# Kernel tuning notes

Measured on AMD Instinct MI355X. Metric: run time of the kernel, lower is better.

The kernel has to match this reference:

```python
import jax, jax.numpy as jnp
import numpy as np

# Brevitas-style fake quantization:
#  - Int8ActPerTensorFloat: signed, symmetric, per-tensor float scale, range [-128, 127]
#  - 4-bit weight, narrow range: [-7, 7]
#  - Int32Bias: quantized at scale s_in * s_w
# Scales are taken from per-tensor abs-max statistics (brevitas stats-based init).

def _round(v):
    return jnp.round(v)

def _fake_quant(v, scale, qmin, qmax):
    return jnp.clip(_round(v / scale), qmin, qmax) * scale


def setup_inputs() -> dict:
    key = jax.random.key(0)
    k1, k2, k3 = jax.random.split(key, 3)
    x = jax.random.normal(k1, (16, 3, 224, 224), dtype=jnp.float32)
    W = jax.random.normal(k2, (128, 3, 3, 3), dtype=jnp.float32) * 0.1
    b = jax.random.normal(k3, (128,), dtype=jnp.float32) * 0.01
    return {"x": x, "W": W, "b": b}


def reference(x, W, b):
    EPS = 1e-8
    # input quant: int8 per-tensor
    s_in = jnp.maximum(jnp.max(jnp.abs(x)) / 127.0, EPS)
    x_q = _fake_quant(x, s_in, -128.0, 127.0)
    # weight quant: 4-bit narrow-range per-tensor
    s_w = jnp.maximum(jnp.max(jnp.abs(W)) / 7.0, EPS)
    w_q = _fake_quant(W, s_w, -7.0, 7.0)
    # bias quant: int32 at scale s_in * s_w
    s_b = s_in * s_w
    b_q = _fake_quant(b, s_b, -2147483648.0, 2147483647.0)
    # conv2d, NCHW x OIHW -> NCHW, stride 1, valid padding (torch default padding=0)
    y = jax.lax.conv_general_dilated(
        x_q, w_q, window_strides=(1, 1), padding="VALID",
        dimension_numbers=("NCHW", "OIHW", "NCHW"))
    y = y + b_q[None, :, None, None]
    # output quant: int8 per-tensor
    s_out = jnp.maximum(jnp.max(jnp.abs(y)) / 127.0, EPS)
    y_q = _fake_quant(y, s_out, -128.0, 127.0)
    return y_q
```

## Files before the change

### kernel.cpp

```cpp
#include <hip/hip_runtime.h>
#include <stdint.h>

#define QEPS 1e-8f


__global__ void k_init(unsigned int* s) { if (threadIdx.x < 4) s[threadIdx.x] = 0u; }

__global__ __launch_bounds__(256) void k_absmax(
    const float4* __restrict__ x, int n4,
    const float* __restrict__ W, int nw,
    unsigned int* __restrict__ s) {
  __shared__ unsigned int red[256];
  const int t = threadIdx.x;
  unsigned int m = 0u;
  const int i = blockIdx.x * 256 + t;
  if (i < n4) {
    float4 v = x[i];
    m =        __float_as_uint(v.x) & 0x7fffffffu;
    m = max(m, __float_as_uint(v.y) & 0x7fffffffu);
    m = max(m, __float_as_uint(v.z) & 0x7fffffffu);
    m = max(m, __float_as_uint(v.w) & 0x7fffffffu);
  }
  red[t] = m;
  __syncthreads();
  for (int off = 128; off > 0; off >>= 1) {
    if (t < off) red[t] = max(red[t], red[t + off]);
    __syncthreads();
  }
  if (t == 0) atomicMax(&s[0], red[0]);

  if (blockIdx.x == 0) {
    unsigned int mw = 0u;
    for (int j = t; j < nw; j += 256)
      mw = max(mw, __float_as_uint(W[j]) & 0x7fffffffu);
    __syncthreads();
    red[t] = mw;
    __syncthreads();
    for (int off = 128; off > 0; off >>= 1) {
      if (t < off) red[t] = max(red[t], red[t + off]);
      __syncthreads();
    }
    if (t == 0) atomicMax(&s[1], red[0]);
  }
}

template<int PASS>
__global__ __launch_bounds__(256, 3) void k_conv(
    const float* __restrict__ x, const float* __restrict__ W,
    const float* __restrict__ b, float* __restrict__ out,
    unsigned int* __restrict__ s) {
  __shared__ __align__(16) float wl[27][128];
  __shared__ __align__(16) float xl[9][132];
  __shared__ float redf[256];

  const int t = threadIdx.x;
  const int lane = t & 15;
  const int oc0 = (t >> 4) * 8;

  const float s_in = fmaxf(__uint_as_float(s[0]) / 127.0f, QEPS);
  const float s_w  = fmaxf(__uint_as_float(s[1]) / 7.0f,  QEPS);
  const float s_b  = s_in * s_w;

  float s_out = 1.0f, h = 1.0f;
  if (PASS == 1) {
    const float vmax = __uint_as_float(s[2]);
    s_out = fmaxf((s_b * vmax) / 127.0f, QEPS);
    h = s_b / s_out;
  }

  for (int i = t; i < 3456; i += 256) {
    const int o = i / 27;
    const int k = i - o * 27;
    float q = rintf(W[i] / s_w);
    wl[k][o] = fminf(fmaxf(q, -7.0f), 7.0f);
  }

  float qb[8];
  #pragma unroll
  for (int cc = 0; cc < 8; ++cc)
    qb[cc] = rintf(b[oc0 + cc] / s_b);

  float vmax_local = 0.0f;

  for (int it = 0; it < 4; ++it) {
    const int tile = blockIdx.x + it * 1776;
    const int owt = tile & 1;
    const int r2 = tile >> 1;
    const int n  = r2 & 15;
    const int oh = r2 >> 4;
    const int ow0 = owt * 128;

    for (int i = t; i < 9 * 132; i += 256) {
      const int row = i / 132;
      const int col = i - row * 132;
      const int c  = row / 3;
      const int kh = row - c * 3;
      const int gcol = ow0 + col;
      float q = 0.0f;
      if (gcol < 224) {
        const float xv = x[((n * 3 + c) * 224 + (oh + kh)) * 224 + gcol];
        q = fminf(fmaxf(rintf(xv / s_in), -128.0f), 127.0f);
      }
      xl[row][col] = q;
    }
    __syncthreads();

    float acc[8][8];
    #pragma unroll
    for (int r = 0; r < 8; ++r)
      #pragma unroll
      for (int cc = 0; cc < 8; ++cc) acc[r][cc] = 0.0f;

    #pragma unroll 1
    for (int ck = 0; ck < 9; ++ck) {
      const float* xr = &xl[ck][lane * 8];
      const float4 a0 = *(const float4*)xr;
      const float4 a1 = *(const float4*)(xr + 4);
      const float4 a2 = *(const float4*)(xr + 8);
      const float xw[12] = {a0.x, a0.y, a0.z, a0.w, a1.x, a1.y, a1.z, a1.w,
                            a2.x, a2.y, a2.z, a2.w};
      #pragma unroll
      for (int kw = 0; kw < 3; ++kw) {
        const float* wp = &wl[ck * 3 + kw][oc0];
        const float4 w0 = *(const float4*)wp;
        const float4 w1 = *(const float4*)(wp + 4);
        const float wv[8] = {w0.x, w0.y, w0.z, w0.w, w1.x, w1.y, w1.z, w1.w};
        #pragma unroll
        for (int r = 0; r < 8; ++r) {
          #pragma unroll
          for (int cc = 0; cc < 8; ++cc)
            acc[r][cc] += xw[r + kw] * wv[cc];
        }
      }
    }

    const int owbase = ow0 + lane * 8;
    const int nv = min(8, 222 - owbase);

    if (PASS == 0) {
      if (nv > 0) {
        #pragma unroll
        for (int r = 0; r < 8; ++r) {
          if (r < nv) {
            #pragma unroll
            for (int cc = 0; cc < 8; ++cc)
              vmax_local = fmaxf(vmax_local, fabsf(acc[r][cc] + qb[cc]));
          }
        }
      }
    } else {
      if (nv > 0) {
        #pragma unroll
        for (int cc = 0; cc < 8; ++cc) {
          float o8[8];
          #pragma unroll
          for (int r = 0; r < 8; ++r) {
            float q = rintf((acc[r][cc] + qb[cc]) * h);
            q = fminf(fmaxf(q, -128.0f), 127.0f);
            o8[r] = q * s_out;
          }
          float* po = out + (((n * 128 + oc0 + cc) * 222 + oh) * 222 + owbase);
          if (nv == 8) {
            if ((oh & 1) == 0) {
              *(float4*)po       = make_float4(o8[0], o8[1], o8[2], o8[3]);
              *(float4*)(po + 4) = make_float4(o8[4], o8[5], o8[6], o8[7]);
            } else {
              *(float2*)po       = make_float2(o8[0], o8[1]);
              *(float2*)(po + 2) = make_float2(o8[2], o8[3]);
              *(float2*)(po + 4) = make_float2(o8[4], o8[5]);
              *(float2*)(po + 6) = make_float2(o8[6], o8[7]);
            }
          } else {
            for (int r = 0; r < nv; ++r) po[r] = o8[r];
          }
        }
      }
    }
    __syncthreads();
  }

  if (PASS == 0) {
    redf[t] = vmax_local;
    __syncthreads();
    for (int off = 128; off > 0; off >>= 1) {
      if (t < off) redf[t] = fmaxf(redf[t], redf[t + off]);
      __syncthreads();
    }
    if (t == 0) atomicMax(&s[2], __float_as_uint(redf[0]));
  }
}

extern "C" void kernel_launch(void* const* d_in, const int* in_sizes, int n_in,
                              void* d_out, int out_size, void* d_ws, size_t ws_size,
                              hipStream_t stream) {
  const float* x = (const float*)d_in[0];
  const float* W = (const float*)d_in[1];
  const float* b = (const float*)d_in[2];
  float* out = (float*)d_out;
  unsigned int* s = (unsigned int*)d_ws;

  k_init<<<1, 64, 0, stream>>>(s);

  const int n4 = in_sizes[0] / 4;
  k_absmax<<<(n4 + 255) / 256, 256, 0, stream>>>(
      (const float4*)x, n4, W, in_sizes[1], s);

  k_conv<0><<<1776, 256, 0, stream>>>(x, W, b, out, s);
  k_conv<1><<<1776, 256, 0, stream>>>(x, W, b, out, s);
}
```

Measured before the change: 634.5 us.

## Use int8 MFMA for quantized conv with prepacked weights and exact integer accumulation

Replaces the fp32 FMA outer-product conv with int8 MFMA (16x16x64) instructions. A new prep kernel quantizes and packs the 4-bit weights into int8 K-major fragments and precomputes the quantized bias. Inputs are quantized to int8 and packed as 9-byte im2col columns in shared memory. The grid changes to one block per 128-wide output row tile instead of four tiles per block. Integer accumulation is exact, so the result should match, but most of the 64-wide K dimension is zero padding. The conv work becomes small, leaving the kernels mostly bound by output stores and launch overhead.

```diff
diff --git a/kernel.cpp b/kernel.cpp
--- a/kernel.cpp
+++ b/kernel.cpp
@@ -1,15 +1,15 @@
 #include <hip/hip_runtime.h>
 #include <stdint.h>
 
+typedef int v4i __attribute__((ext_vector_type(4)));
+
 #define QEPS 1e-8f
 
 
 __global__ void k_init(unsigned int* s) { if (threadIdx.x < 4) s[threadIdx.x] = 0u; }
 
 __global__ __launch_bounds__(256) void k_absmax(
-    const float4* __restrict__ x, int n4,
-    const float* __restrict__ W, int nw,
-    unsigned int* __restrict__ s) {
+    const float4* __restrict__ x, int n4, unsigned int* __restrict__ s) {
   __shared__ unsigned int red[256];
   const int t = threadIdx.x;
   unsigned int m = 0u;
@@ -28,165 +28,170 @@
     __syncthreads();
   }
   if (t == 0) atomicMax(&s[0], red[0]);
-
-  if (blockIdx.x == 0) {
-    unsigned int mw = 0u;
-    for (int j = t; j < nw; j += 256)
-      mw = max(mw, __float_as_uint(W[j]) & 0x7fffffffu);
+}
+
+__global__ __launch_bounds__(128) void k_prep(
+    const float* __restrict__ W, const float* __restrict__ b,
+    unsigned int* __restrict__ s, int* __restrict__ wB, float* __restrict__ qb) {
+  __shared__ float red[128];
+  const int t = threadIdx.x;
+  float w27[27];
+  float m = 0.0f;
+  #pragma unroll
+  for (int k = 0; k < 27; ++k) { w27[k] = W[t * 27 + k]; m = fmaxf(m, fabsf(w27[k])); }
+  red[t] = m;
+  __syncthreads();
+  for (int off = 64; off > 0; off >>= 1) {
+    if (t < off) red[t] = fmaxf(red[t], red[t + off]);
     __syncthreads();
-    red[t] = mw;
+  }
+  const float wmax = red[0];
+  if (t == 0) s[1] = __float_as_uint(wmax);
+  const float s_w  = fmaxf(wmax / 7.0f, QEPS);
+  const float s_in = fmaxf(__uint_as_float(s[0]) / 127.0f, QEPS);
+
+  int q[27];
+  #pragma unroll
+  for (int k = 0; k < 27; ++k) {
+    float v = rintf(w27[k] / s_w);
+    q[k] = (int)fminf(fmaxf(v, -7.0f), 7.0f);
+  }
+  #pragma unroll
+  for (int qd = 0; qd < 4; ++qd) {
+    #pragma unroll
+    for (int w = 0; w < 4; ++w) {
+      int word = 0;
+      #pragma unroll
+      for (int bi = 0; bi < 4; ++bi) {
+        const int j = 4 * w + bi;
+        const int val = (qd < 3 && j < 9) ? q[j * 3 + qd] : 0;
+        word |= (val & 0xff) << (8 * bi);
+      }
+      wB[t * 16 + qd * 4 + w] = word;
+    }
+  }
+  qb[t] = rintf(b[t] / (s_in * s_w));
+}
+
+template<int PASS>
+__global__ __launch_bounds__(256, 3) void k_conv(
+    const float* __restrict__ x, const int* __restrict__ wB,
+    const float* __restrict__ qb, float* __restrict__ out,
+    unsigned int* __restrict__ s) {
+  __shared__ __align__(16) int xcol[132 * 4];
+  __shared__ int redi[256];
+
+  const int t = threadIdx.x;
+  const int owt = blockIdx.x & 1;
+  const int r2 = blockIdx.x >> 1;
+  const int n  = r2 & 15;
+  const int oh = r2 >> 4;
+  const int ow0 = owt * 128;
+
+  const float s_in = fmaxf(__uint_as_float(s[0]) / 127.0f, QEPS);
+
+  if (t < 131) {
+    const int gcol = ow0 + t;
+    int qv[9];
+    if (gcol < 224) {
+      #pragma unroll
+      for (int r = 0; r < 9; ++r) {
+        const int c = r / 3, kh = r - c * 3;
+        const float xv = x[((n * 3 + c) * 224 + (oh + kh)) * 224 + gcol];
+        qv[r] = (int)fminf(fmaxf(rintf(xv / s_in), -128.0f), 127.0f);
+      }
+    } else {
+      #pragma unroll
+      for (int r = 0; r < 9; ++r) qv[r] = 0;
+    }
+    const int w0 = (qv[0] & 0xff) | (qv[1] & 0xff) << 8 | (qv[2] & 0xff) << 16 | (qv[3] & 0xff) << 24;
+    const int w1 = (qv[4] & 0xff) | (qv[5] & 0xff) << 8 | (qv[6] & 0xff) << 16 | (qv[7] & 0xff) << 24;
+    const int w2 = (qv[8] & 0xff);
+    ((v4i*)xcol)[t] = (v4i){w0, w1, w2, 0};
+  }
+
+  const int lane = t & 63;
+  const int wv   = t >> 6;
+  const int l15  = lane & 15;
+  const int quad = lane >> 4;
+
+  v4i bfr[8];
+  int qbi[8];
+  #pragma unroll
+  for (int nt = 0; nt < 8; ++nt) {
+    bfr[nt] = ((const v4i*)wB)[(nt * 16 + l15) * 4 + quad];
+    qbi[nt] = (int)qb[nt * 16 + l15];
+  }
+
+  __syncthreads();
+
+  v4i afr[2];
+  #pragma unroll
+  for (int mt = 0; mt < 2; ++mt)
+    afr[mt] = ((const v4i*)xcol)[(2 * wv + mt) * 16 + l15 + quad];
+
+  v4i acc[2][8];
+  #pragma unroll
+  for (int mt = 0; mt < 2; ++mt)
+    #pragma unroll
+    for (int nt = 0; nt < 8; ++nt) acc[mt][nt] = (v4i){0, 0, 0, 0};
+
+  #pragma unroll
+  for (int mt = 0; mt < 2; ++mt)
+    #pragma unroll
+    for (int nt = 0; nt < 8; ++nt)
+      acc[mt][nt] = __builtin_amdgcn_mfma_i32_16x16x64_i8(afr[mt], bfr[nt], acc[mt][nt], 0, 0, 0);
+
+  if (PASS == 0) {
+    int vm = 0;
+    #pragma unroll
+    for (int mt = 0; mt < 2; ++mt) {
+      const int owb = ow0 + (2 * wv + mt) * 16 + quad * 4;
+      #pragma unroll
+      for (int nt = 0; nt < 8; ++nt) {
+        #pragma unroll
+        for (int r = 0; r < 4; ++r) {
+          if (owb + r < 222) {
+            const int v = acc[mt][nt][r] + qbi[nt];
+            vm = max(vm, v < 0 ? -v : v);
+          }
+        }
+      }
+    }
+    redi[t] = vm;
     __syncthreads();
     for (int off = 128; off > 0; off >>= 1) {
-      if (t < off) red[t] = max(red[t], red[t + off]);
+      if (t < off) redi[t] = max(redi[t], redi[t + off]);
       __syncthreads();
     }
-    if (t == 0) atomicMax(&s[1], red[0]);
-  }
-}
-
-template<int PASS>
-__global__ __launch_bounds__(256, 3) void k_conv(
-    const float* __restrict__ x, const float* __restrict__ W,
-    const float* __restrict__ b, float* __restrict__ out,
-    unsigned int* __restrict__ s) {
-  __shared__ __align__(16) float wl[27][128];
-  __shared__ __align__(16) float xl[9][132];
-  __shared__ float redf[256];
-
-  const int t = threadIdx.x;
-  const int lane = t & 15;
-  const int oc0 = (t >> 4) * 8;
-
-  const float s_in = fmaxf(__uint_as_float(s[0]) / 127.0f, QEPS);
-  const float s_w  = fmaxf(__uint_as_float(s[1]) / 7.0f,  QEPS);
-  const float s_b  = s_in * s_w;
-
-  float s_out = 1.0f, h = 1.0f;
-  if (PASS == 1) {
-    const float vmax = __uint_as_float(s[2]);
-    s_out = fmaxf((s_b * vmax) / 127.0f, QEPS);
-    h = s_b / s_out;
-  }
-
-  for (int i = t; i < 3456; i += 256) {
-    const int o = i / 27;
-    const int k = i - o * 27;
-    float q = rintf(W[i] / s_w);
-    wl[k][o] = fminf(fmaxf(q, -7.0f), 7.0f);
-  }
-
-  float qb[8];
-  #pragma unroll
-  for (int cc = 0; cc < 8; ++cc)
-    qb[cc] = rintf(b[oc0 + cc] / s_b);
-
-  float vmax_local = 0.0f;
-
-  for (int it = 0; it < 4; ++it) {
-    const int tile = blockIdx.x + it * 1776;
-    const int owt = tile & 1;
-    const int r2 = tile >> 1;
-    const int n  = r2 & 15;
-    const int oh = r2 >> 4;
-    const int ow0 = owt * 128;
-
-    for (int i = t; i < 9 * 132; i += 256) {
-      const int row = i / 132;
-      const int col = i - row * 132;
-      const int c  = row / 3;
-      const int kh = row - c * 3;
-      const int gcol = ow0 + col;
-      float q = 0.0f;
-      if (gcol < 224) {
-        const float xv = x[((n * 3 + c) * 224 + (oh + kh)) * 224 + gcol];
-        q = fminf(fmaxf(rintf(xv / s_in), -128.0f), 127.0f);
-      }
-      xl[row][col] = q;
-    }
-    __syncthreads();
-
-    float acc[8][8];
-    #pragma unroll
-    for (int r = 0; r < 8; ++r)
-      #pragma unroll
-      for (int cc = 0; cc < 8; ++cc) acc[r][cc] = 0.0f;
-
-    #pragma unroll 1
-    for (int ck = 0; ck < 9; ++ck) {
-      const float* xr = &xl[ck][lane * 8];
-      const float4 a0 = *(const float4*)xr;
-      const float4 a1 = *(const float4*)(xr + 4);
-      const float4 a2 = *(const float4*)(xr + 8);
-      const float xw[12] = {a0.x, a0.y, a0.z, a0.w, a1.x, a1.y, a1.z, a1.w,
-                            a2.x, a2.y, a2.z, a2.w};
-      #pragma unroll
-      for (int kw = 0; kw < 3; ++kw) {
-        const float* wp = &wl[ck * 3 + kw][oc0];
-        const float4 w0 = *(const float4*)wp;
-        const float4 w1 = *(const float4*)(wp + 4);
-        const float wv[8] = {w0.x, w0.y, w0.z, w0.w, w1.x, w1.y, w1.z, w1.w};
+    if (t == 0) atomicMax(&s[2], (unsigned int)redi[0]);
+  } else {
+    const int vmax = (int)s[2];
+    const float s_w  = fmaxf(__uint_as_float(s[1]) / 7.0f, QEPS);
+    const float s_b  = s_in * s_w;
+    const float s_out = fmaxf((s_b * (float)vmax) / 127.0f, QEPS);
+    const float h = s_b / s_out;
+    #pragma unroll
+    for (int mt = 0; mt < 2; ++mt) {
+      const int owb = ow0 + (2 * wv + mt) * 16 + quad * 4;
+      if (owb < 222) {
         #pragma unroll
-        for (int r = 0; r < 8; ++r) {
+        for (int nt = 0; nt < 8; ++nt) {
+          const int oc = nt * 16 + l15;
+          float o4[4];
           #pragma unroll
-          for (int cc = 0; cc < 8; ++cc)
-            acc[r][cc] += xw[r + kw] * wv[cc];
+          for (int r = 0; r < 4; ++r) {
+            const float vf = (float)(acc[mt][nt][r] + qbi[nt]);
+            float q = rintf(vf * h);
+            q = fminf(fmaxf(q, -128.0f), 127.0f);
+            o4[r] = q * s_out;
+          }
+          float* p = out + ((n * 128 + oc) * 49284 + oh * 222 + owb);
+          *(float2*)p = make_float2(o4[0], o4[1]);
+          if (owb + 2 < 222) *(float2*)(p + 2) = make_float2(o4[2], o4[3]);
         }
       }
     }
-
-    const int owbase = ow0 + lane * 8;
-    const int nv = min(8, 222 - owbase);
-
-    if (PASS == 0) {
-      if (nv > 0) {
-        #pragma unroll
-        for (int r = 0; r < 8; ++r) {
-          if (r < nv) {
-            #pragma unroll
-            for (int cc = 0; cc < 8; ++cc)
-              vmax_local = fmaxf(vmax_local, fabsf(acc[r][cc] + qb[cc]));
-          }
-        }
-      }
-    } else {
-      if (nv > 0) {
-        #pragma unroll
-        for (int cc = 0; cc < 8; ++cc) {
-          float o8[8];
-          #pragma unroll
-          for (int r = 0; r < 8; ++r) {
-            float q = rintf((acc[r][cc] + qb[cc]) * h);
-            q = fminf(fmaxf(q, -128.0f), 127.0f);
-            o8[r] = q * s_out;
-          }
-          float* po = out + (((n * 128 + oc0 + cc) * 222 + oh) * 222 + owbase);
-          if (nv == 8) {
-            if ((oh & 1) == 0) {
-              *(float4*)po       = make_float4(o8[0], o8[1], o8[2], o8[3]);
-              *(float4*)(po + 4) = make_float4(o8[4], o8[5], o8[6], o8[7]);
-            } else {
-              *(float2*)po       = make_float2(o8[0], o8[1]);
-              *(float2*)(po + 2) = make_float2(o8[2], o8[3]);
-              *(float2*)(po + 4) = make_float2(o8[4], o8[5]);
-              *(float2*)(po + 6) = make_float2(o8[6], o8[7]);
-            }
-          } else {
-            for (int r = 0; r < nv; ++r) po[r] = o8[r];
-          }
-        }
-      }
-    }
-    __syncthreads();
-  }
-
-  if (PASS == 0) {
-    redf[t] = vmax_local;
-    __syncthreads();
-    for (int off = 128; off > 0; off >>= 1) {
-      if (t < off) redf[t] = fmaxf(redf[t], redf[t + off]);
-      __syncthreads();
-    }
-    if (t == 0) atomicMax(&s[2], __float_as_uint(redf[0]));
   }
 }
 
@@ -197,14 +202,19 @@
   const float* W = (const float*)d_in[1];
   const float* b = (const float*)d_in[2];
   float* out = (float*)d_out;
+
   unsigned int* s = (unsigned int*)d_ws;
+  int*   wB = (int*)((char*)d_ws + 256);
+  float* qb = (float*)((char*)d_ws + 256 + 8192);
 
   k_init<<<1, 64, 0, stream>>>(s);
 
   const int n4 = in_sizes[0] / 4;
-  k_absmax<<<(n4 + 255) / 256, 256, 0, stream>>>(
-      (const float4*)x, n4, W, in_sizes[1], s);
-
-  k_conv<0><<<1776, 256, 0, stream>>>(x, W, b, out, s);
-  k_conv<1><<<1776, 256, 0, stream>>>(x, W, b, out, s);
-}
+  k_absmax<<<(n4 + 255) / 256, 256, 0, stream>>>((const float4*)x, n4, s);
+
+  k_prep<<<1, 128, 0, stream>>>(W, b, s, wB, qb);
+
+  const int nblk = 2 * 16 * 222;
+  k_conv<0><<<nblk, 256, 0, stream>>>(x, wB, qb, out, s);
+  k_conv<1><<<nblk, 256, 0, stream>>>(x, wB, qb, out, s);
+}
```

Measured after the change: 666.9 us. 5.1% more time.
